# Kernel tuning notes

Hardware: AMD Instinct MI355X
Metric: run time of the kernel (lower is better)

## Reference

```python
import jax, jax.numpy as jnp
import numpy as np
from math import sqrt

B, S, F, H, FF, L = 16, 512, 512, 8, 2048, 3
HEAD_DIM = F // H
LN_EPS = 1e-5


def setup_inputs() -> dict:
    key = jax.random.key(0)
    ks = iter(jax.random.split(key, 80))

    def nrm(shape, scale=0.02):
        return jax.random.normal(next(ks), shape, jnp.float32) * scale

    inp = {
        "embedding": jax.random.normal(next(ks), (B, S, F), jnp.float32),
        "lengths": jax.random.randint(next(ks), (B,), 1, S + 1, dtype=jnp.int32),
    }
    for p in ("enc", "dec"):
        inp[p + "_wqkv"] = nrm((L, 3, F, F))
        inp[p + "_bqkv"] = nrm((L, 3, F))
        inp[p + "_wo"] = nrm((L, F, F))
        inp[p + "_bo"] = nrm((L, F))
        inp[p + "_ln1_g"] = jnp.ones((L, F), jnp.float32)
        inp[p + "_ln1_b"] = jnp.zeros((L, F), jnp.float32)
        inp[p + "_ff_w1"] = nrm((L, F, FF))
        inp[p + "_ff_b1"] = nrm((L, FF))
        inp[p + "_ff_w2"] = nrm((L, FF, F))
        inp[p + "_ff_b2"] = nrm((L, F))
        inp[p + "_ln2_g"] = jnp.ones((L, F), jnp.float32)
        inp[p + "_ln2_b"] = jnp.zeros((L, F), jnp.float32)
    inp["ptr_w_q"] = nrm((F,), 1.0)
    inp["ptr_w_k"] = nrm((F,), 1.0)
    return inp


def _ln(x, g, b):
    mu = x.mean(-1, keepdims=True)
    var = ((x - mu) ** 2).mean(-1, keepdims=True)
    return (x - mu) / jnp.sqrt(var + LN_EPS) * g + b


def _mha(q_in, kv_in, wqkv, bqkv, wo, bo, mask):
    # q_in [b,sq,f], kv_in [b,sk,f], mask broadcastable to [b,h,sq,sk] (True = masked)
    b, sq, f = q_in.shape
    q = q_in @ wqkv[0] + bqkv[0]
    k = kv_in @ wqkv[1] + bqkv[1]
    v = kv_in @ wqkv[2] + bqkv[2]

    def split(t):
        return t.reshape(t.shape[0], t.shape[1], H, HEAD_DIM).transpose(0, 2, 1, 3)

    q, k, v = split(q), split(k), split(v)  # [b,h,s,dh]
    scores = jnp.einsum("bhqd,bhkd->bhqk", q, k) / sqrt(HEAD_DIM)
    scores = jnp.where(mask, jnp.finfo(scores.dtype).min, scores)
    attn = jax.nn.softmax(scores, axis=-1)
    out = jnp.einsum("bhqk,bhkd->bhqd", attn, v)
    out = out.transpose(0, 2, 1, 3).reshape(b, sq, f)
    return out @ wo + bo


def _layer(x, mem, mask, wqkv, bqkv, wo, bo, ln1_g, ln1_b, w1, b1, w2, b2, ln2_g, ln2_b):
    x = _ln(x + _mha(x, mem, wqkv, bqkv, wo, bo, mask), ln1_g, ln1_b)
    ff = jax.nn.gelu(x @ w1 + b1, approximate=False) @ w2 + b2
    return _ln(x + ff, ln2_g, ln2_b)


def _forward(embedding, lengths,
             enc_wqkv, enc_bqkv, enc_wo, enc_bo, enc_ln1_g, enc_ln1_b,
             enc_ff_w1, enc_ff_b1, enc_ff_w2, enc_ff_b2, enc_ln2_g, enc_ln2_b,
             dec_wqkv, dec_bqkv, dec_wo, dec_bo, dec_ln1_g, dec_ln1_b,
             dec_ff_w1, dec_ff_b1, dec_ff_w2, dec_ff_b2, dec_ln2_g, dec_ln2_b,
             ptr_w_q, ptr_w_k):
    b, s, f = embedding.shape
    pos = jnp.arange(s)
    key_mask = pos[None, :] >= lengths[:, None]  # [b,s] True = padded

    # ---- encoder (self-attn with key padding mask) ----
    enc_mask = key_mask[:, None, None, :]  # [b,1,1,s]
    x = embedding
    for i in range(L):
        x = _layer(x, x, enc_mask,
                   enc_wqkv[i], enc_bqkv[i], enc_wo[i], enc_bo[i],
                   enc_ln1_g[i], enc_ln1_b[i],
                   enc_ff_w1[i], enc_ff_b1[i], enc_ff_w2[i], enc_ff_b2[i],
                   enc_ln2_g[i], enc_ln2_b[i])
    memory = x

    # ---- decoder: all timesteps batched (no recurrent state in original loop) ----
    # query t attends keys j < min(t, len); t=0 is overridden with zeros below
    # (key 0 left unmasked for t=0 only to keep softmax finite).
    t = jnp.arange(s)
    limit = jnp.minimum(jnp.maximum(t, 1)[None, :], lengths[:, None])  # [b,sq]
    dec_mask = (pos[None, None, :] >= limit[:, :, None])[:, None, :, :]  # [b,1,sq,sk]
    y = embedding
    for i in range(L):
        y = _layer(y, memory, dec_mask,
                   dec_wqkv[i], dec_bqkv[i], dec_wo[i], dec_bo[i],
                   dec_ln1_g[i], dec_ln1_b[i],
                   dec_ff_w1[i], dec_ff_b1[i], dec_ff_w2[i], dec_ff_b2[i],
                   dec_ln2_g[i], dec_ln2_b[i])

    # ---- pointer logits ----
    wq = y @ ptr_w_q        # [b, sq]
    wk = memory @ ptr_w_k   # [b, sk]
    ptr = jax.nn.sigmoid((wq[:, None, :] + wk[:, :, None]) / sqrt(f))  # [b, sk, sq]
    return jnp.where(t[None, None, :] == 0, 0.0, ptr)


def reference(embedding, lengths,
              enc_wqkv, enc_bqkv, enc_wo, enc_bo, enc_ln1_g, enc_ln1_b,
              enc_ff_w1, enc_ff_b1, enc_ff_w2, enc_ff_b2, enc_ln2_g, enc_ln2_b,
              dec_wqkv, dec_bqkv, dec_wo, dec_bo, dec_ln1_g, dec_ln1_b,
              dec_ff_w1, dec_ff_b1, dec_ff_w2, dec_ff_b2, dec_ln2_g, dec_ln2_b,
              ptr_w_q, ptr_w_k):
    return _forward(embedding, lengths,
                    enc_wqkv, enc_bqkv, enc_wo, enc_bo, enc_ln1_g, enc_ln1_b,
                    enc_ff_w1, enc_ff_b1, enc_ff_w2, enc_ff_b2, enc_ln2_g, enc_ln2_b,
                    dec_wqkv, dec_bqkv, dec_wo, dec_bo, dec_ln1_g, dec_ln1_b,
                    dec_ff_w1, dec_ff_b1, dec_ff_w2, dec_ff_b2, dec_ln2_g, dec_ln2_b,
                    ptr_w_q, ptr_w_k)
```

## Files before the change

kernel.cpp:

```cpp
#include <hip/hip_runtime.h>
#include <hip/hip_bf16.h>
#include <math.h>

#define TB 16
#define TS 512
#define TF 512
#define TH 8
#define TFF 2048
#define TL 3

typedef unsigned short u16;
typedef short bf16x8 __attribute__((ext_vector_type(8)));
typedef float f32x4 __attribute__((ext_vector_type(4)));

__device__ __forceinline__ u16 f2b(float f) {
    __hip_bfloat16 h = __float2bfloat16(f);
    return *reinterpret_cast<u16*>(&h);
}

__device__ __forceinline__ void gload_lds16(const void* g, void* l) {
    __builtin_amdgcn_global_load_lds(
        (const __attribute__((address_space(1))) unsigned int*)g,
        (__attribute__((address_space(3))) unsigned int*)l, 16, 0, 0);
}

__global__ __launch_bounds__(256) void k_transpose_w(
    const float* __restrict__ src, u16* __restrict__ dst, int K, int N)
{
    __shared__ float tile[32][33];
    const int z = blockIdx.z;
    src += (size_t)z * K * N;
    dst += (size_t)z * K * N;
    const int n0 = blockIdx.x * 32, k0 = blockIdx.y * 32;
    const int tx = threadIdx.x & 31, ty = threadIdx.x >> 5;
    #pragma unroll
    for (int i = 0; i < 32; i += 8)
        tile[ty + i][tx] = src[(size_t)(k0 + ty + i) * N + n0 + tx];
    __syncthreads();
    #pragma unroll
    for (int i = 0; i < 32; i += 8)
        dst[(size_t)(n0 + ty + i) * K + k0 + tx] = f2b(tile[tx][ty + i]);
}

__global__ __launch_bounds__(256) void k_cvt(
    const float* __restrict__ src, float* __restrict__ d32,
    u16* __restrict__ d16, int n4)
{
    const int i = blockIdx.x * 256 + threadIdx.x;
    if (i >= n4) return;
    float4 v = ((const float4*)src)[i];
    if (d32) ((float4*)d32)[i] = v;
    ushort4 p;
    p.x = f2b(v.x); p.y = f2b(v.y); p.z = f2b(v.z); p.w = f2b(v.w);
    ((ushort4*)d16)[i] = p;
}

template<int EPI, int BN>
__global__ __launch_bounds__(256) void k_gemm(
    const u16* __restrict__ A, const u16* __restrict__ A2, int asplit,
    const u16* __restrict__ BT,
    const float* __restrict__ bias, const float* __restrict__ resid,
    u16* __restrict__ outb, float* __restrict__ outf,
    u16* __restrict__ out_k, u16* __restrict__ out_v,
    int N, int K, int ldo, int coloff)
{
    __shared__ __align__(16) u16 As[2][128 * 64];
    __shared__ __align__(16) u16 Bs[2][BN * 64];
    const int gx = gridDim.x;
    int bid = blockIdx.y * gx + blockIdx.x;
    const int cpx = (gx * gridDim.y) >> 3;
    bid = (bid & 7) * cpx + (bid >> 3);
    const int bn = bid % gx, bm = bid / gx;

    const int t = threadIdx.x;
    const int w = t >> 6, l = t & 63;
    const int wm = w >> 1, wn = w & 1;
    const int lhi = l >> 4, llo = l & 15;
    constexpr int NFR = BN / 64 * 2;

    f32x4 acc[4][NFR];
    #pragma unroll
    for (int m = 0; m < 4; ++m)
        #pragma unroll
        for (int n = 0; n < NFR; ++n)
            acc[m][n] = f32x4{0.f, 0.f, 0.f, 0.f};

    const u16* Asrc = (bn * BN < asplit) ? A : A2;

    const int lr = l >> 3;
    const int lcz = ((l & 7) ^ lr) * 8;
    const u16* Ag = Asrc + (size_t)(bm * 128 + w * 8 + lr) * K + lcz;
    const u16* Bg = BT + (size_t)(bn * BN + w * 8 + lr) * K + lcz;

    auto stage = [&](int buf, int kofs) {
        #pragma unroll
        for (int ro = 0; ro < 4; ++ro)
            gload_lds16(Ag + (size_t)ro * 32 * K + kofs, &As[buf][(w * 8 + ro * 32) * 64]);
        #pragma unroll
        for (int ro = 0; ro < BN / 32; ++ro)
            gload_lds16(Bg + (size_t)ro * 32 * K + kofs, &Bs[buf][(w * 8 + ro * 32) * 64]);
    };

    const int NT = K >> 6;
    stage(0, 0);
    for (int kt = 0; kt < NT; ++kt) {
        const int cur = kt & 1;
        if (kt + 1 < NT) {
            stage(cur ^ 1, (kt + 1) << 6);
            if constexpr (BN == 128) asm volatile("s_waitcnt vmcnt(8)" ::: "memory");
            else                     asm volatile("s_waitcnt vmcnt(6)" ::: "memory");
        } else {
            asm volatile("s_waitcnt vmcnt(0)" ::: "memory");
        }
        __builtin_amdgcn_s_barrier();
        __builtin_amdgcn_sched_barrier(0);
        #pragma unroll
        for (int kk = 0; kk < 2; ++kk) {
            bf16x8 af[4], bfr[NFR];
            #pragma unroll
            for (int m = 0; m < 4; ++m) {
                const int row = wm * 64 + m * 16 + llo;
                const int ch = (kk * 4 + lhi) ^ (llo & 7);
                af[m] = *(const bf16x8*)(&As[cur][row * 64 + ch * 8]);
            }
            #pragma unroll
            for (int n = 0; n < NFR; ++n) {
                const int row = wn * (BN / 2) + n * 16 + llo;
                const int ch = (kk * 4 + lhi) ^ (llo & 7);
                bfr[n] = *(const bf16x8*)(&Bs[cur][row * 64 + ch * 8]);
            }
            #pragma unroll
            for (int m = 0; m < 4; ++m)
                #pragma unroll
                for (int n = 0; n < NFR; ++n)
                    acc[m][n] = __builtin_amdgcn_mfma_f32_16x16x32_bf16(
                        af[m], bfr[n], acc[m][n], 0, 0, 0);
        }
        __builtin_amdgcn_sched_barrier(0);
        __builtin_amdgcn_s_barrier();
    }

    const int colb = bn * BN + wn * (BN / 2);
    const int rowb = bm * 128 + wm * 64 + lhi * 4;
    const int c0 = coloff + bn * BN;

    if (EPI == 3 && c0 >= 1024) {
        u16* tb = &As[0][0] + w * 4096;
        #pragma unroll
        for (int n = 0; n < 4; ++n) {
            const int dl = n * 16 + llo;
            const float bv = bias[colb + n * 16 + llo];
            #pragma unroll
            for (int m = 0; m < 4; ++m) {
                ushort4 pk;
                #pragma unroll
                for (int r = 0; r < 4; ++r)
                    ((u16*)&pk)[r] = f2b(acc[m][n][r] + bv);
                const int slc = m * 2 + (lhi >> 1);
                const int addr = dl * 64 + ((slc ^ (dl & 7)) << 3) + ((lhi & 1) << 2);
                *(ushort4*)(tb + addr) = pk;
            }
        }
        asm volatile("s_waitcnt lgkmcnt(0)" ::: "memory");
        __builtin_amdgcn_sched_barrier(0);
        const int sbase = bm * 128 + wm * 64;
        const int bidx = sbase >> 9;
        const int srem = sbase & 511;
        const int hh = ((c0 + wn * 64) >> 6) & 7;
        u16* vo = out_v + ((size_t)bidx * 8 + hh) * 32768 + srem;
        const int cchunk = l & 7;
        #pragma unroll
        for (int rr = 0; rr < 8; ++rr) {
            const int dl2 = (l >> 3) + rr * 8;
            const int ch = cchunk ^ (dl2 & 7);
            bf16x8 vv = *(const bf16x8*)(tb + dl2 * 64 + ch * 8);
            *(bf16x8*)(vo + (size_t)dl2 * 512 + cchunk * 8) = vv;
        }
        return;
    }

    #pragma unroll
    for (int n = 0; n < NFR; ++n) {
        const int col = colb + n * 16 + llo;
        const float bv = bias[col];
        #pragma unroll
        for (int m = 0; m < 4; ++m) {
            const int row = rowb + m * 16;
            if (EPI == 3) {
                float vv[4];
                #pragma unroll
                for (int r = 0; r < 4; ++r) vv[r] = acc[m][n][r] + bv;
                const int c = coloff + col;
                if ((c >> 9) == 0) {
                    #pragma unroll
                    for (int r = 0; r < 4; ++r)
                        outb[(size_t)(row + r) * 512 + c] = f2b(vv[r]);
                } else {
                    const int hh = (c >> 6) & 7, d = c & 63;
                    #pragma unroll
                    for (int r = 0; r < 4; ++r) {
                        const int rr = row + r;
                        out_k[((size_t)(rr >> 9) * 8 + hh) * 32768 + (rr & 511) * 64 + d] = f2b(vv[r]);
                    }
                }
            } else {
                #pragma unroll
                for (int r = 0; r < 4; ++r) {
                    float v = acc[m][n][r] + bv;
                    const size_t off = (size_t)(row + r) * ldo + coloff + col;
                    if (EPI == 0) {
                        outb[off] = f2b(v);
                    } else if (EPI == 1) {
                        v = 0.5f * v * (1.f + erff(v * 0.70710678118654752f));
                        outb[off] = f2b(v);
                    } else {
                        outf[off] = v + resid[off];
                    }
                }
            }
        }
    }
}

template<int DEC>
__global__ __launch_bounds__(256) void k_attn(
    const u16* __restrict__ qb, const u16* __restrict__ kc,
    const u16* __restrict__ vtp, const int* __restrict__ lengths,
    u16* __restrict__ out)
{
    __shared__ __align__(16) u16 Ks[2][64 * 64];
    __shared__ __align__(16) u16 Vs[2][64 * 64];
    __shared__ __align__(16) u16 plds[4][16][64];
    __shared__ float alds[4][16];
    __shared__ float llds[4][16];
    const int qt = blockIdx.x;
    const int bh = blockIdx.y;
    const int b = bh >> 3;
    const int h = bh & 7;
    const int t = threadIdx.x, w = t >> 6, l = t & 63;
    const int lhi = l >> 4, llo = l & 15;
    const int len = lengths[b];
    const int qrow0 = qt * 64 + w * 16;
    const int q = qrow0 + llo;

    const u16* qp = qb + (size_t)(b * TS + q) * 512 + h * 64 + lhi * 8;
    bf16x8 qf0 = *(const bf16x8*)(qp);
    bf16x8 qf1 = *(const bf16x8*)(qp + 32);

    const u16* kb = kc  + (size_t)bh * 32768;
    const u16* vb = vtp + (size_t)bh * 32768;

    const int qlim = DEC ? min(max(q, 1), len) : len;
    const int limb = DEC ? min(qt * 64 + 63, len) : len;
    const int ktend = (limb + 63) >> 6;

    f32x4 o[4];
    #pragma unroll
    for (int g = 0; g < 4; ++g) o[g] = f32x4{0.f, 0.f, 0.f, 0.f};
    float mrun = -1e30f, lrun = 0.f;

    const float SC = 0.18033688011112042f;

    const int sr = w * 8 + (l >> 3);
    const int sc = (((l & 7) ^ (sr & 7)) << 3);
    auto stage = [&](int buf, int ktt) {
        gload_lds16(kb + ((ktt * 64 + sr) << 6) + sc,        &Ks[buf][(w * 8) * 64]);
        gload_lds16(kb + ((ktt * 64 + 32 + sr) << 6) + sc,   &Ks[buf][(32 + w * 8) * 64]);
        gload_lds16(vb + (size_t)sr * 512 + ktt * 64 + sc,   &Vs[buf][(w * 8) * 64]);
        gload_lds16(vb + (size_t)(32 + sr) * 512 + ktt * 64 + sc, &Vs[buf][(32 + w * 8) * 64]);
    };

    stage(0, 0);
    for (int kt = 0; kt < ktend; ++kt) {
        const int cur = kt & 1;
        if (kt + 1 < ktend) {
            stage(cur ^ 1, kt + 1);
            asm volatile("s_waitcnt vmcnt(4)" ::: "memory");
        } else {
            asm volatile("s_waitcnt vmcnt(0)" ::: "memory");
        }
        __builtin_amdgcn_s_barrier();
        __builtin_amdgcn_sched_barrier(0);

        bf16x8 kf[4][2], vf[4][2];
        #pragma unroll
        for (int g = 0; g < 4; ++g) {
            const int row = g * 16 + llo;
            const int x = row & 7;
            kf[g][0] = *(const bf16x8*)&Ks[cur][row * 64 + ((lhi) ^ x) * 8];
            kf[g][1] = *(const bf16x8*)&Ks[cur][row * 64 + ((4 + lhi) ^ x) * 8];
            vf[g][0] = *(const bf16x8*)&Vs[cur][row * 64 + ((lhi) ^ x) * 8];
            vf[g][1] = *(const bf16x8*)&Vs[cur][row * 64 + ((4 + lhi) ^ x) * 8];
        }
        f32x4 s[4];
        #pragma unroll
        for (int g = 0; g < 4; ++g) {
            s[g] = f32x4{0.f, 0.f, 0.f, 0.f};
            s[g] = __builtin_amdgcn_mfma_f32_16x16x32_bf16(kf[g][0], qf0, s[g], 0, 0, 0);
            s[g] = __builtin_amdgcn_mfma_f32_16x16x32_bf16(kf[g][1], qf1, s[g], 0, 0, 0);
        }
        #pragma unroll
        for (int g = 0; g < 4; ++g) {
            const int key = kt * 64 + g * 16 + lhi * 4;
            #pragma unroll
            for (int r = 0; r < 4; ++r)
                s[g][r] = (key + r < qlim) ? s[g][r] * SC : -1e30f;
        }
        float tm = fmaxf(fmaxf(fmaxf(s[0][0], s[0][1]), fmaxf(s[0][2], s[0][3])),
                         fmaxf(fmaxf(s[1][0], s[1][1]), fmaxf(s[1][2], s[1][3])));
        tm = fmaxf(tm, fmaxf(fmaxf(fmaxf(s[2][0], s[2][1]), fmaxf(s[2][2], s[2][3])),
                             fmaxf(fmaxf(s[3][0], s[3][1]), fmaxf(s[3][2], s[3][3]))));
        tm = fmaxf(tm, __shfl_xor(tm, 16));
        tm = fmaxf(tm, __shfl_xor(tm, 32));
        const float mnew = fmaxf(mrun, tm);
        const float alpha = exp2f(mrun - mnew);
        mrun = mnew;
        float rs = 0.f;
        ushort4 pk[4];
        #pragma unroll
        for (int g = 0; g < 4; ++g) {
            #pragma unroll
            for (int r = 0; r < 4; ++r) {
                const float p = exp2f(s[g][r] - mnew);
                rs += p;
                ((u16*)&pk[g])[r] = f2b(p);
            }
        }
        rs += __shfl_xor(rs, 16);
        rs += __shfl_xor(rs, 32);
        lrun = lrun * alpha + rs;
        if (lhi == 0) alds[w][llo] = alpha;
        #pragma unroll
        for (int g = 0; g < 4; ++g) {
            const int chw = (g * 2 + (lhi >> 1)) ^ (llo & 7);
            *(ushort4*)((char*)&plds[w][0][0] + llo * 128 + chw * 16 + (lhi & 1) * 8) = pk[g];
        }
        const float4 av = *(const float4*)&alds[w][lhi * 4];
        #pragma unroll
        for (int g = 0; g < 4; ++g) {
            o[g][0] *= av.x; o[g][1] *= av.y; o[g][2] *= av.z; o[g][3] *= av.w;
        }
        #pragma unroll
        for (int ks = 0; ks < 2; ++ks) {
            const int chr = (ks * 4 + lhi) ^ (llo & 7);
            bf16x8 pa = *(const bf16x8*)((const char*)&plds[w][0][0] + llo * 128 + chr * 16);
            #pragma unroll
            for (int g = 0; g < 4; ++g)
                o[g] = __builtin_amdgcn_mfma_f32_16x16x32_bf16(pa, vf[g][ks], o[g], 0, 0, 0);
        }
        __builtin_amdgcn_sched_barrier(0);
        __builtin_amdgcn_s_barrier();
    }

    if (lhi == 0) llds[w][llo] = 1.f / lrun;
    __builtin_amdgcn_s_waitcnt(0);
    const float4 linv = *(const float4*)&llds[w][lhi * 4];
    #pragma unroll
    for (int g = 0; g < 4; ++g) {
        const int d = h * 64 + g * 16 + llo;
        #pragma unroll
        for (int r = 0; r < 4; ++r) {
            const int qq = qrow0 + lhi * 4 + r;
            out[(size_t)(b * TS + qq) * 512 + d] = f2b(o[g][r] * ((const float*)&linv)[r]);
        }
    }
}

__global__ __launch_bounds__(256) void k_ln(
    const float* __restrict__ in, const float* __restrict__ gam,
    const float* __restrict__ bet, float* __restrict__ o32, u16* __restrict__ o16)
{
    const int row = blockIdx.x * 4 + (threadIdx.x >> 6);
    const int l = threadIdx.x & 63;
    const float* p = in + (size_t)row * 512 + l * 8;
    float x[8];
    *(float4*)&x[0] = *(const float4*)p;
    *(float4*)&x[4] = *(const float4*)(p + 4);
    float s = x[0] + x[1] + x[2] + x[3] + x[4] + x[5] + x[6] + x[7];
    #pragma unroll
    for (int off = 32; off; off >>= 1) s += __shfl_xor(s, off);
    const float mu = s * (1.f / 512.f);
    float v = 0.f;
    #pragma unroll
    for (int i = 0; i < 8; ++i) { const float d = x[i] - mu; v += d * d; }
    #pragma unroll
    for (int off = 32; off; off >>= 1) v += __shfl_xor(v, off);
    const float rstd = rsqrtf(v * (1.f / 512.f) + 1e-5f);
    float gg[8], bb[8];
    *(float4*)&gg[0] = *(const float4*)(gam + l * 8);
    *(float4*)&gg[4] = *(const float4*)(gam + l * 8 + 4);
    *(float4*)&bb[0] = *(const float4*)(bet + l * 8);
    *(float4*)&bb[4] = *(const float4*)(bet + l * 8 + 4);
    float y[8];
    #pragma unroll
    for (int i = 0; i < 8; ++i) y[i] = (x[i] - mu) * rstd * gg[i] + bb[i];
    float* op = o32 + (size_t)row * 512 + l * 8;
    *(float4*)op = *(float4*)&y[0];
    *(float4*)(op + 4) = *(float4*)&y[4];
    ushort4 pk0, pk1;
    pk0.x = f2b(y[0]); pk0.y = f2b(y[1]); pk0.z = f2b(y[2]); pk0.w = f2b(y[3]);
    pk1.x = f2b(y[4]); pk1.y = f2b(y[5]); pk1.z = f2b(y[6]); pk1.w = f2b(y[7]);
    ushort4* o16p = (ushort4*)(o16 + (size_t)row * 512 + l * 8);
    o16p[0] = pk0; o16p[1] = pk1;
}

__global__ __launch_bounds__(256) void k_rowdot(
    const float* __restrict__ x, const float* __restrict__ wv, float* __restrict__ out)
{
    const int row = blockIdx.x * 4 + (threadIdx.x >> 6);
    const int l = threadIdx.x & 63;
    const float* p = x + (size_t)row * 512 + l * 8;
    float4 a = *(const float4*)p;
    float4 b = *(const float4*)(p + 4);
    float4 wa = *(const float4*)(wv + l * 8);
    float4 wb = *(const float4*)(wv + l * 8 + 4);
    float s = a.x * wa.x + a.y * wa.y + a.z * wa.z + a.w * wa.w
            + b.x * wb.x + b.y * wb.y + b.z * wb.z + b.w * wb.w;
    #pragma unroll
    for (int off = 32; off; off >>= 1) s += __shfl_xor(s, off);
    if (l == 0) out[row] = s;
}

__global__ __launch_bounds__(256) void k_ptr_out(
    const float* __restrict__ wq, const float* __restrict__ wk, float* __restrict__ out)
{
    const int bi = blockIdx.x;
    const int b = bi >> 9;
    const float wki = wk[bi];
    #pragma unroll
    for (int j = threadIdx.x; j < 512; j += 256) {
        float r = 0.f;
        if (j != 0) {
            const float z = (wq[b * 512 + j] + wki) * 0.044194173824159216f;
            r = 1.f / (1.f + __expf(-z));
        }
        out[(size_t)bi * 512 + j] = r;
    }
}

extern "C" void kernel_launch(void* const* d_in, const int* in_sizes, int n_in,
                              void* d_out, int out_size, void* d_ws, size_t ws_size,
                              hipStream_t stream)
{
    const float* emb = (const float*)d_in[0];
    const int* lengths = (const int*)d_in[1];
    struct Pw {
        const float *wqkv, *bqkv, *wo, *bo, *ln1g, *ln1b, *w1, *b1, *w2, *b2, *ln2g, *ln2b;
    } pp[2];
    for (int p = 0; p < 2; ++p) {
        const int base = 2 + p * 12;
        pp[p].wqkv = (const float*)d_in[base + 0];
        pp[p].bqkv = (const float*)d_in[base + 1];
        pp[p].wo   = (const float*)d_in[base + 2];
        pp[p].bo   = (const float*)d_in[base + 3];
        pp[p].ln1g = (const float*)d_in[base + 4];
        pp[p].ln1b = (const float*)d_in[base + 5];
        pp[p].w1   = (const float*)d_in[base + 6];
        pp[p].b1   = (const float*)d_in[base + 7];
        pp[p].w2   = (const float*)d_in[base + 8];
        pp[p].b2   = (const float*)d_in[base + 9];
        pp[p].ln2g = (const float*)d_in[base + 10];
        pp[p].ln2b = (const float*)d_in[base + 11];
    }
    const float* pwq = (const float*)d_in[26];
    const float* pwk = (const float*)d_in[27];

    char* ws = (char*)d_ws;
    auto alloc = [&](size_t bytes) {
        char* p = ws;
        ws += (bytes + 255) & ~(size_t)255;
        return p;
    };
    u16* wqkvT[2], *woT[2], *w1T[2], *w2T[2];
    for (int p = 0; p < 2; ++p) {
        wqkvT[p] = (u16*)alloc((size_t)TL * 1536 * 512 * 2);
        woT[p]   = (u16*)alloc((size_t)TL * 512 * 512 * 2);
        w1T[p]   = (u16*)alloc((size_t)TL * 2048 * 512 * 2);
        w2T[p]   = (u16*)alloc((size_t)TL * 512 * 2048 * 2);
    }
    const size_t MR = (size_t)TB * TS;
    float* x32   = (float*)alloc(MR * 512 * 4);
    u16*   x16   = (u16*)alloc(MR * 512 * 2);
    float* mem32 = (float*)alloc(MR * 512 * 4);
    u16*   mem16 = (u16*)alloc(MR * 512 * 2);
    u16*   qbuf  = (u16*)alloc(MR * 512 * 2);
    u16*   kcb   = (u16*)alloc((size_t)TB * TH * 512 * 64 * 2);
    u16*   vtb   = (u16*)alloc((size_t)TB * TH * 64 * 512 * 2);
    u16*   att16 = (u16*)alloc(MR * 512 * 2);
    float* preln = (float*)alloc(MR * 512 * 4);
    u16*   h16   = (u16*)alloc(MR * 2048 * 2);
    float* wqb   = (float*)alloc(MR * 4);
    float* wkb   = (float*)alloc(MR * 4);

    for (int p = 0; p < 2; ++p) {
        k_transpose_w<<<dim3(16, 16, 9), 256, 0, stream>>>(pp[p].wqkv, wqkvT[p], 512, 512);
        k_transpose_w<<<dim3(16, 16, 3), 256, 0, stream>>>(pp[p].wo, woT[p], 512, 512);
        k_transpose_w<<<dim3(64, 16, 3), 256, 0, stream>>>(pp[p].w1, w1T[p], 512, 2048);
        k_transpose_w<<<dim3(16, 64, 3), 256, 0, stream>>>(pp[p].w2, w2T[p], 2048, 512);
    }

    const int n4 = (int)(MR * 512 / 4);
    k_cvt<<<4096, 256, 0, stream>>>(emb, x32, x16, n4);

    for (int i = 0; i < TL; ++i) {
        k_gemm<3, 128><<<dim3(12, 64), 256, 0, stream>>>(
            x16, x16, 1536, wqkvT[0] + (size_t)i * 1536 * 512, pp[0].bqkv + i * 1536,
            nullptr, qbuf, nullptr, kcb, vtb, 1536, 512, 1536, 0);
        k_attn<0><<<dim3(8, 128), 256, 0, stream>>>(qbuf, kcb, vtb, lengths, att16);
        k_gemm<2, 64><<<dim3(8, 64), 256, 0, stream>>>(
            att16, att16, 512, woT[0] + (size_t)i * 512 * 512, pp[0].bo + i * 512,
            x32, nullptr, preln, nullptr, nullptr, 512, 512, 512, 0);
        k_ln<<<2048, 256, 0, stream>>>(preln, pp[0].ln1g + i * 512, pp[0].ln1b + i * 512, x32, x16);
        k_gemm<1, 128><<<dim3(16, 64), 256, 0, stream>>>(
            x16, x16, 2048, w1T[0] + (size_t)i * 2048 * 512, pp[0].b1 + i * 2048,
            nullptr, h16, nullptr, nullptr, nullptr, 2048, 512, 2048, 0);
        k_gemm<2, 64><<<dim3(8, 64), 256, 0, stream>>>(
            h16, h16, 512, w2T[0] + (size_t)i * 512 * 2048, pp[0].b2 + i * 512,
            x32, nullptr, preln, nullptr, nullptr, 512, 2048, 512, 0);
        if (i == TL - 1)
            k_ln<<<2048, 256, 0, stream>>>(preln, pp[0].ln2g + i * 512, pp[0].ln2b + i * 512, mem32, mem16);
        else
            k_ln<<<2048, 256, 0, stream>>>(preln, pp[0].ln2g + i * 512, pp[0].ln2b + i * 512, x32, x16);
    }
    k_cvt<<<4096, 256, 0, stream>>>(emb, x32, x16, n4);

    for (int i = 0; i < TL; ++i) {
        k_gemm<3, 128><<<dim3(12, 64), 256, 0, stream>>>(
            x16, mem16, 512, wqkvT[1] + (size_t)i * 1536 * 512, pp[1].bqkv + i * 1536,
            nullptr, qbuf, nullptr, kcb, vtb, 1536, 512, 1536, 0);
        k_attn<1><<<dim3(8, 128), 256, 0, stream>>>(qbuf, kcb, vtb, lengths, att16);
        k_gemm<2, 64><<<dim3(8, 64), 256, 0, stream>>>(
            att16, att16, 512, woT[1] + (size_t)i * 512 * 512, pp[1].bo + i * 512,
            x32, nullptr, preln, nullptr, nullptr, 512, 512, 512, 0);
        k_ln<<<2048, 256, 0, stream>>>(preln, pp[1].ln1g + i * 512, pp[1].ln1b + i * 512, x32, x16);
        k_gemm<1, 128><<<dim3(16, 64), 256, 0, stream>>>(
            x16, x16, 2048, w1T[1] + (size_t)i * 2048 * 512, pp[1].b1 + i * 2048,
            nullptr, h16, nullptr, nullptr, nullptr, 2048, 512, 2048, 0);
        k_gemm<2, 64><<<dim3(8, 64), 256, 0, stream>>>(
            h16, h16, 512, w2T[1] + (size_t)i * 512 * 2048, pp[1].b2 + i * 512,
            x32, nullptr, preln, nullptr, nullptr, 512, 2048, 512, 0);
        k_ln<<<2048, 256, 0, stream>>>(preln, pp[1].ln2g + i * 512, pp[1].ln2b + i * 512, x32, x16);
    }

    k_rowdot<<<2048, 256, 0, stream>>>(x32, pwq, wqb);
    k_rowdot<<<2048, 256, 0, stream>>>(mem32, pwk, wkb);
    k_ptr_out<<<TB * TS, 256, 0, stream>>>(wqb, wkb, (float*)d_out);
}
```

Before: 1.023 ms.

## Restructure GEMM to 8-wave 512-thread blocks with wider N tiles and split-phase prefetch

Replaces the 4-wave GEMM with an 8-wave, 512-thread kernel whose N tile is doubled (256 for QKV/FFN1, 128 for output projections), so fewer blocks each reuse the loaded A tile across more columns. The main loop loads all LDS fragments up front and splits the MFMAs into two halves. The next-next tile's global-to-LDS load is issued between the halves, behind a barrier, so the copy overlaps the second half of the math. MFMA sections are raised in priority with s_setprio. The trade-off is fewer blocks per GEMM, which may underfill the GPU's compute units on the smaller output-projection GEMMs, plus more register pressure per wave.

Measured after the change: 977.5 us. 4.4% less time.

```diff
diff --git a/kernel.cpp b/kernel.cpp
--- a/kernel.cpp
+++ b/kernel.cpp
@@ -56,7 +56,7 @@
 }
 
 template<int EPI, int BN>
-__global__ __launch_bounds__(256) void k_gemm(
+__global__ __launch_bounds__(512, 1) void k_g8(
     const u16* __restrict__ A, const u16* __restrict__ A2, int asplit,
     const u16* __restrict__ BT,
     const float* __restrict__ bias, const float* __restrict__ resid,
@@ -64,8 +64,12 @@
     u16* __restrict__ out_k, u16* __restrict__ out_v,
     int N, int K, int ldo, int coloff)
 {
-    __shared__ __align__(16) u16 As[2][128 * 64];
-    __shared__ __align__(16) u16 Bs[2][BN * 64];
+    constexpr int NFB = BN / 64;
+    constexpr int NL = 2 + BN / 64;
+    __shared__ __align__(16) u16 SH[2 * 128 * 64 + 2 * BN * 64];
+    u16* Asm = SH;
+    u16* Bsm = SH + 2 * 128 * 64;
+
     const int gx = gridDim.x;
     int bid = blockIdx.y * gx + blockIdx.x;
     const int cpx = (gx * gridDim.y) >> 3;
@@ -74,113 +78,129 @@
 
     const int t = threadIdx.x;
     const int w = t >> 6, l = t & 63;
-    const int wm = w >> 1, wn = w & 1;
+    const int wm = w >> 2, wn = w & 3;
     const int lhi = l >> 4, llo = l & 15;
-    constexpr int NFR = BN / 64 * 2;
-
-    f32x4 acc[4][NFR];
+
+    f32x4 acc[4][NFB];
     #pragma unroll
     for (int m = 0; m < 4; ++m)
         #pragma unroll
-        for (int n = 0; n < NFR; ++n)
+        for (int n = 0; n < NFB; ++n)
             acc[m][n] = f32x4{0.f, 0.f, 0.f, 0.f};
 
     const u16* Asrc = (bn * BN < asplit) ? A : A2;
-
     const int lr = l >> 3;
     const int lcz = ((l & 7) ^ lr) * 8;
     const u16* Ag = Asrc + (size_t)(bm * 128 + w * 8 + lr) * K + lcz;
     const u16* Bg = BT + (size_t)(bn * BN + w * 8 + lr) * K + lcz;
 
-    auto stage = [&](int buf, int kofs) {
-        #pragma unroll
-        for (int ro = 0; ro < 4; ++ro)
-            gload_lds16(Ag + (size_t)ro * 32 * K + kofs, &As[buf][(w * 8 + ro * 32) * 64]);
-        #pragma unroll
-        for (int ro = 0; ro < BN / 32; ++ro)
-            gload_lds16(Bg + (size_t)ro * 32 * K + kofs, &Bs[buf][(w * 8 + ro * 32) * 64]);
+    auto stage = [&](int buf, int tt) {
+        const int kofs = tt << 6;
+        gload_lds16(Ag + kofs,          Asm + buf * 8192 + (w * 8) * 64);
+        gload_lds16(Ag + 64 * K + kofs, Asm + buf * 8192 + (64 + w * 8) * 64);
+        #pragma unroll
+        for (int i = 0; i < BN / 64; ++i)
+            gload_lds16(Bg + (size_t)i * 64 * K + kofs,
+                        Bsm + buf * (BN * 64) + (i * 64 + w * 8) * 64);
     };
 
     const int NT = K >> 6;
     stage(0, 0);
-    for (int kt = 0; kt < NT; ++kt) {
-        const int cur = kt & 1;
-        if (kt + 1 < NT) {
-            stage(cur ^ 1, (kt + 1) << 6);
-            if constexpr (BN == 128) asm volatile("s_waitcnt vmcnt(8)" ::: "memory");
-            else                     asm volatile("s_waitcnt vmcnt(6)" ::: "memory");
+    stage(1, 1);
+    for (int tt = 0; tt < NT; ++tt) {
+        const int cur = tt & 1;
+        if (tt + 1 < NT) {
+            if constexpr (BN == 256) asm volatile("s_waitcnt vmcnt(6)" ::: "memory");
+            else                     asm volatile("s_waitcnt vmcnt(4)" ::: "memory");
         } else {
             asm volatile("s_waitcnt vmcnt(0)" ::: "memory");
         }
         __builtin_amdgcn_s_barrier();
         __builtin_amdgcn_sched_barrier(0);
-        #pragma unroll
-        for (int kk = 0; kk < 2; ++kk) {
-            bf16x8 af[4], bfr[NFR];
-            #pragma unroll
-            for (int m = 0; m < 4; ++m) {
-                const int row = wm * 64 + m * 16 + llo;
-                const int ch = (kk * 4 + lhi) ^ (llo & 7);
-                af[m] = *(const bf16x8*)(&As[cur][row * 64 + ch * 8]);
+
+        bf16x8 af[4][2], bfr[NFB][2];
+        #pragma unroll
+        for (int m = 0; m < 4; ++m) {
+            const int row = wm * 64 + m * 16 + llo;
+            const int x = row & 7;
+            af[m][0] = *(const bf16x8*)(Asm + cur * 8192 + row * 64 + ((lhi) ^ x) * 8);
+            af[m][1] = *(const bf16x8*)(Asm + cur * 8192 + row * 64 + ((4 + lhi) ^ x) * 8);
+        }
+        #pragma unroll
+        for (int n = 0; n < NFB; ++n) {
+            const int row = wn * (BN / 4) + n * 16 + llo;
+            const int x = row & 7;
+            bfr[n][0] = *(const bf16x8*)(Bsm + cur * (BN * 64) + row * 64 + ((lhi) ^ x) * 8);
+            bfr[n][1] = *(const bf16x8*)(Bsm + cur * (BN * 64) + row * 64 + ((4 + lhi) ^ x) * 8);
+        }
+        asm volatile("s_waitcnt lgkmcnt(0)" ::: "memory");
+        __builtin_amdgcn_sched_barrier(0);
+        __builtin_amdgcn_s_setprio(1);
+        #pragma unroll
+        for (int m = 0; m < 2; ++m)
+            #pragma unroll
+            for (int n = 0; n < NFB; ++n) {
+                acc[m][n] = __builtin_amdgcn_mfma_f32_16x16x32_bf16(af[m][0], bfr[n][0], acc[m][n], 0, 0, 0);
+                acc[m][n] = __builtin_amdgcn_mfma_f32_16x16x32_bf16(af[m][1], bfr[n][1], acc[m][n], 0, 0, 0);
             }
-            #pragma unroll
-            for (int n = 0; n < NFR; ++n) {
-                const int row = wn * (BN / 2) + n * 16 + llo;
-                const int ch = (kk * 4 + lhi) ^ (llo & 7);
-                bfr[n] = *(const bf16x8*)(&Bs[cur][row * 64 + ch * 8]);
-            }
-            #pragma unroll
-            for (int m = 0; m < 4; ++m)
-                #pragma unroll
-                for (int n = 0; n < NFR; ++n)
-                    acc[m][n] = __builtin_amdgcn_mfma_f32_16x16x32_bf16(
-                        af[m], bfr[n], acc[m][n], 0, 0, 0);
-        }
+        __builtin_amdgcn_s_setprio(0);
         __builtin_amdgcn_sched_barrier(0);
         __builtin_amdgcn_s_barrier();
-    }
-
-    const int colb = bn * BN + wn * (BN / 2);
+        if (tt + 2 < NT) stage(cur, tt + 2);
+        __builtin_amdgcn_s_setprio(1);
+        #pragma unroll
+        for (int m = 2; m < 4; ++m)
+            #pragma unroll
+            for (int n = 0; n < NFB; ++n) {
+                acc[m][n] = __builtin_amdgcn_mfma_f32_16x16x32_bf16(af[m][0], bfr[n][0], acc[m][n], 0, 0, 0);
+                acc[m][n] = __builtin_amdgcn_mfma_f32_16x16x32_bf16(af[m][1], bfr[n][1], acc[m][n], 0, 0, 0);
+            }
+        __builtin_amdgcn_s_setprio(0);
+    }
+
+    const int colb = bn * BN + wn * (BN / 4);
     const int rowb = bm * 128 + wm * 64 + lhi * 4;
-    const int c0 = coloff + bn * BN;
-
-    if (EPI == 3 && c0 >= 1024) {
-        u16* tb = &As[0][0] + w * 4096;
-        #pragma unroll
-        for (int n = 0; n < 4; ++n) {
-            const int dl = n * 16 + llo;
-            const float bv = bias[colb + n * 16 + llo];
-            #pragma unroll
-            for (int m = 0; m < 4; ++m) {
-                ushort4 pk;
+    const int c0w = coloff + colb;
+
+    if constexpr (EPI == 3 && BN == 256) {
+        if (c0w >= 1024) {
+            u16* tb = SH + w * 4096;
+            #pragma unroll
+            for (int n = 0; n < 4; ++n) {
+                const int dl = n * 16 + llo;
+                const float bv = bias[colb + n * 16 + llo];
                 #pragma unroll
-                for (int r = 0; r < 4; ++r)
-                    ((u16*)&pk)[r] = f2b(acc[m][n][r] + bv);
-                const int slc = m * 2 + (lhi >> 1);
-                const int addr = dl * 64 + ((slc ^ (dl & 7)) << 3) + ((lhi & 1) << 2);
-                *(ushort4*)(tb + addr) = pk;
+                for (int m = 0; m < 4; ++m) {
+                    ushort4 pk;
+                    #pragma unroll
+                    for (int r = 0; r < 4; ++r)
+                        ((u16*)&pk)[r] = f2b(acc[m][n][r] + bv);
+                    const int slc = m * 2 + (lhi >> 1);
+                    const int addr = dl * 64 + ((slc ^ (dl & 7)) << 3) + ((lhi & 1) << 2);
+                    *(ushort4*)(tb + addr) = pk;
+                }
             }
-        }
-        asm volatile("s_waitcnt lgkmcnt(0)" ::: "memory");
-        __builtin_amdgcn_sched_barrier(0);
-        const int sbase = bm * 128 + wm * 64;
-        const int bidx = sbase >> 9;
-        const int srem = sbase & 511;
-        const int hh = ((c0 + wn * 64) >> 6) & 7;
-        u16* vo = out_v + ((size_t)bidx * 8 + hh) * 32768 + srem;
-        const int cchunk = l & 7;
-        #pragma unroll
-        for (int rr = 0; rr < 8; ++rr) {
-            const int dl2 = (l >> 3) + rr * 8;
-            const int ch = cchunk ^ (dl2 & 7);
-            bf16x8 vv = *(const bf16x8*)(tb + dl2 * 64 + ch * 8);
-            *(bf16x8*)(vo + (size_t)dl2 * 512 + cchunk * 8) = vv;
-        }
-        return;
-    }
-
-    #pragma unroll
-    for (int n = 0; n < NFR; ++n) {
+            asm volatile("s_waitcnt lgkmcnt(0)" ::: "memory");
+            __builtin_amdgcn_sched_barrier(0);
+            const int sbase = bm * 128 + wm * 64;
+            const int bidx = sbase >> 9;
+            const int srem = sbase & 511;
+            const int hh = (c0w >> 6) & 7;
+            u16* vo = out_v + ((size_t)bidx * 8 + hh) * 32768 + srem;
+            const int cchunk = l & 7;
+            #pragma unroll
+            for (int rr = 0; rr < 8; ++rr) {
+                const int dl2 = (l >> 3) + rr * 8;
+                const int ch = cchunk ^ (dl2 & 7);
+                bf16x8 vv = *(const bf16x8*)(tb + dl2 * 64 + ch * 8);
+                *(bf16x8*)(vo + (size_t)dl2 * 512 + cchunk * 8) = vv;
+            }
+            return;
+        }
+    }
+
+    #pragma unroll
+    for (int n = 0; n < NFB; ++n) {
         const int col = colb + n * 16 + llo;
         const float bv = bias[col];
         #pragma unroll
@@ -503,18 +523,18 @@
     k_cvt<<<4096, 256, 0, stream>>>(emb, x32, x16, n4);
 
     for (int i = 0; i < TL; ++i) {
-        k_gemm<3, 128><<<dim3(12, 64), 256, 0, stream>>>(
+        k_g8<3, 256><<<dim3(6, 64), 512, 0, stream>>>(
             x16, x16, 1536, wqkvT[0] + (size_t)i * 1536 * 512, pp[0].bqkv + i * 1536,
             nullptr, qbuf, nullptr, kcb, vtb, 1536, 512, 1536, 0);
         k_attn<0><<<dim3(8, 128), 256, 0, stream>>>(qbuf, kcb, vtb, lengths, att16);
-        k_gemm<2, 64><<<dim3(8, 64), 256, 0, stream>>>(
+        k_g8<2, 128><<<dim3(4, 64), 512, 0, stream>>>(
             att16, att16, 512, woT[0] + (size_t)i * 512 * 512, pp[0].bo + i * 512,
             x32, nullptr, preln, nullptr, nullptr, 512, 512, 512, 0);
         k_ln<<<2048, 256, 0, stream>>>(preln, pp[0].ln1g + i * 512, pp[0].ln1b + i * 512, x32, x16);
-        k_gemm<1, 128><<<dim3(16, 64), 256, 0, stream>>>(
+        k_g8<1, 256><<<dim3(8, 64), 512, 0, stream>>>(
             x16, x16, 2048, w1T[0] + (size_t)i * 2048 * 512, pp[0].b1 + i * 2048,
             nullptr, h16, nullptr, nullptr, nullptr, 2048, 512, 2048, 0);
-        k_gemm<2, 64><<<dim3(8, 64), 256, 0, stream>>>(
+        k_g8<2, 128><<<dim3(4, 64), 512, 0, stream>>>(
             h16, h16, 512, w2T[0] + (size_t)i * 512 * 2048, pp[0].b2 + i * 512,
             x32, nullptr, preln, nullptr, nullptr, 512, 2048, 512, 0);
         if (i == TL - 1)
@@ -525,18 +545,18 @@
     k_cvt<<<4096, 256, 0, stream>>>(emb, x32, x16, n4);
 
     for (int i = 0; i < TL; ++i) {
-        k_gemm<3, 128><<<dim3(12, 64), 256, 0, stream>>>(
+        k_g8<3, 256><<<dim3(6, 64), 512, 0, stream>>>(
             x16, mem16, 512, wqkvT[1] + (size_t)i * 1536 * 512, pp[1].bqkv + i * 1536,
             nullptr, qbuf, nullptr, kcb, vtb, 1536, 512, 1536, 0);
         k_attn<1><<<dim3(8, 128), 256, 0, stream>>>(qbuf, kcb, vtb, lengths, att16);
-        k_gemm<2, 64><<<dim3(8, 64), 256, 0, stream>>>(
+        k_g8<2, 128><<<dim3(4, 64), 512, 0, stream>>>(
             att16, att16, 512, woT[1] + (size_t)i * 512 * 512, pp[1].bo + i * 512,
             x32, nullptr, preln, nullptr, nullptr, 512, 512, 512, 0);
         k_ln<<<2048, 256, 0, stream>>>(preln, pp[1].ln1g + i * 512, pp[1].ln1b + i * 512, x32, x16);
-        k_gemm<1, 128><<<dim3(16, 64), 256, 0, stream>>>(
+        k_g8<1, 256><<<dim3(8, 64), 512, 0, stream>>>(
             x16, x16, 2048, w1T[1] + (size_t)i * 2048 * 512, pp[1].b1 + i * 2048,
             nullptr, h16, nullptr, nullptr, nullptr, 2048, 512, 2048, 0);
-        k_gemm<2, 64><<<dim3(8, 64), 256, 0, stream>>>(
+        k_g8<2, 128><<<dim3(4, 64), 512, 0, stream>>>(
             h16, h16, 512, w2T[1] + (size_t)i * 512 * 2048, pp[1].b2 + i * 512,
             x32, nullptr, preln, nullptr, nullptr, 512, 2048, 512, 0);
         k_ln<<<2048, 256, 0, stream>>>(preln, pp[1].ln2g + i * 512, pp[1].ln2b + i * 512, x32, x16);
```
